# Performance work log

Hardware: AMD Instinct MI355X
Metric: run time of the kernel (lower is better)

The kernel has to match this reference:

```python
import jax, jax.numpy as jnp
import numpy as np

NUM_GROUPS = 16
MINIS_PER_GROUP = 16
MINIS_PER_TOK = 4
HIDDEN = 8192
N_TOKENS = 8192


def setup_inputs() -> dict:
    key = jax.random.key(0)
    k1, k2, k3 = jax.random.split(key, 3)
    hidden_states = jax.random.normal(k1, (N_TOKENS, HIDDEN), dtype=jnp.float32)
    # nn.Linear weight: [num_groups, hidden]
    group_gate_w = jax.random.normal(k2, (NUM_GROUPS, HIDDEN), dtype=jnp.float32) * 0.02
    # mini_gates parameter: [num_groups, hidden, minis_per_group]
    mini_gates = jax.random.normal(k3, (NUM_GROUPS, HIDDEN, MINIS_PER_GROUP), dtype=jnp.float32) * 0.02
    return {"hidden_states": hidden_states, "group_gate_w": group_gate_w, "mini_gates": mini_gates}


def reference(hidden_states, group_gate_w, mini_gates):
    # Tier 1: group gate
    group_logits = hidden_states @ group_gate_w.T                      # [N, G]
    group_probs = jax.nn.softmax(group_logits.astype(jnp.float32), axis=-1)
    top_group_probs = jnp.max(group_probs, axis=-1)                    # [N]
    top_group_indices = jnp.argmax(group_probs, axis=-1)               # [N]

    # Tier 2: per-token mini-gate. Instead of gathering a huge [N, H, E]
    # tensor (as the torch code does), compute logits for ALL groups
    # ([N, G, E] is tiny) and select the chosen group's row — same math.
    all_mini_logits = jnp.einsum('nh,ghe->nge', hidden_states, mini_gates)  # [N, G, E]
    mini_logits = jnp.take_along_axis(
        all_mini_logits, top_group_indices[:, None, None], axis=1
    )[:, 0, :]                                                         # [N, E]
    mini_probs = jax.nn.softmax(mini_logits.astype(jnp.float32), axis=-1)

    topk_mini_probs, topk_mini_indices = jax.lax.top_k(mini_probs, MINIS_PER_TOK)
    final_probs = top_group_probs[:, None] * topk_mini_probs
    final_probs = final_probs / jnp.sum(final_probs, axis=-1, keepdims=True)

    global_expert_indices = top_group_indices[:, None] * MINIS_PER_GROUP + topk_mini_indices

    group_aux_loss = jnp.sum(jnp.mean(group_probs, axis=0) ** 2)
    mini_aux_loss = jnp.sum(jnp.mean(mini_probs, axis=0) ** 2)
    total_aux_loss = group_aux_loss + mini_aux_loss

    return (final_probs.astype(hidden_states.dtype), global_expert_indices, total_aux_loss)
```

## Files before the change

kernel.cpp:

```cpp
#include <hip/hip_runtime.h>
#include <math.h>

#define N_TOK 8192
#define HID   8192
#define NG    16
#define NE    16
#define KC    256
#define NCHUNK (HID / KC)
#define TPB   16
#define TPW   2

#define OFF_CNT   0u
#define OFF_GSUM  64u
#define OFF_ESUM  128u
#define OFF_NTIL  192u
#define ZERO_BYTES 256u
#define OFF_BUCK  256u
#define OFF_SCHED (OFF_BUCK + NG*N_TOK*4)
#define OFF_MGT   (OFF_SCHED + 2048*4)

__device__ __forceinline__ void glds16(const float* gp, float* lp) {
    __builtin_amdgcn_global_load_lds(
        (const __attribute__((address_space(1))) void*)gp,
        (__attribute__((address_space(3))) void*)lp, 16, 0, 0);
}

#define RS_ROUND(o, half)                                                 \
  {                                                                       \
    const bool hi_ = (lane & (o)) != 0;                                   \
    _Pragma("unroll")                                                     \
    for (int i_ = 0; i_ < (half); ++i_) {                                 \
      float s_ = hi_ ? acc[i_] : acc[i_ + (half)];                        \
      float r_ = __shfl_xor(s_, (o));                                     \
      acc[i_] = (hi_ ? acc[i_ + (half)] : acc[i_]) + r_;                  \
    }                                                                     \
  }

__global__ __launch_bounds__(512, 4) void k_group(
    const float* __restrict__ hid, const float* __restrict__ gw,
    int* __restrict__ cnt, int* __restrict__ buckets, float* __restrict__ gsum)
{
    __shared__ float Wl[2][NG * KC];
    const int tid  = threadIdx.x;
    const int lane = tid & 63;
    const int wv   = tid >> 6;
    const int t0   = blockIdx.x * TPB + wv * TPW;
    const float* __restrict__ a0 = hid + (size_t)t0 * HID;

    #pragma unroll
    for (int j = 0; j < 2; ++j) {
        int g = wv * 2 + j;
        glds16(gw + (size_t)g * HID + 4 * lane, &Wl[0][g * KC]);
    }
    float4 areg[TPW];
    #pragma unroll
    for (int t = 0; t < TPW; ++t)
        areg[t] = *(const float4*)&a0[(size_t)t * HID + 4 * lane];

    float acc[32];
    #pragma unroll
    for (int i = 0; i < 32; ++i) acc[i] = 0.f;

    for (int c = 0; c < NCHUNK; ++c) {
        __syncthreads();
        float4 aC[TPW];
        #pragma unroll
        for (int t = 0; t < TPW; ++t) aC[t] = areg[t];
        if (c + 1 < NCHUNK) {
            const int kb = (c + 1) * KC;
            #pragma unroll
            for (int j = 0; j < 2; ++j) {
                int g = wv * 2 + j;
                glds16(gw + (size_t)g * HID + kb + 4 * lane, &Wl[(c + 1) & 1][g * KC]);
            }
            #pragma unroll
            for (int t = 0; t < TPW; ++t)
                areg[t] = *(const float4*)&a0[(size_t)t * HID + kb + 4 * lane];
        }
        const float* Wc = &Wl[c & 1][0];
        #pragma unroll
        for (int g = 0; g < NG; ++g) {
            float4 w = *(const float4*)&Wc[g * KC + 4 * lane];
            #pragma unroll
            for (int t = 0; t < TPW; ++t) {
                acc[t*16+g] = fmaf(aC[t].x, w.x, acc[t*16+g]);
                acc[t*16+g] = fmaf(aC[t].y, w.y, acc[t*16+g]);
                acc[t*16+g] = fmaf(aC[t].z, w.z, acc[t*16+g]);
                acc[t*16+g] = fmaf(aC[t].w, w.w, acc[t*16+g]);
            }
        }
    }

    #pragma unroll
    for (int i = 0; i < 32; ++i) acc[i] += __shfl_xor(acc[i], 32);
    RS_ROUND(16, 16) RS_ROUND(8, 8) RS_ROUND(4, 4) RS_ROUND(2, 2) RS_ROUND(1, 1)
    float v = acc[0];
    float mx = v;
    #pragma unroll
    for (int o = 8; o; o >>= 1) mx = fmaxf(mx, __shfl_xor(mx, o));
    float p = expf(v - mx);
    float s = p;
    #pragma unroll
    for (int o = 8; o; o >>= 1) s += __shfl_xor(s, o);
    p /= s;
    float x = p;
    x += __shfl_xor(x, 16);
    if (lane < 16) unsafeAtomicAdd(&gsum[lane], x);
    int gi = lane & 15; float bv = v;
    #pragma unroll
    for (int o = 8; o; o >>= 1) {
        float ov = __shfl_xor(bv, o);
        int   og = __shfl_xor(gi, o);
        if (ov > bv || (ov == bv && og < gi)) { bv = ov; gi = og; }
    }
    if (lane < 32 && (lane & 15) == 0) {
        int t = t0 + (lane >> 4);
        int pos = atomicAdd(&cnt[gi], 1);
        buckets[gi * N_TOK + pos] = t;
    }
}

__global__ __launch_bounds__(256) void k_tr(
    const float* __restrict__ mg, float* __restrict__ mgT)
{
    const int g  = blockIdx.x >> 7;
    const int kb = (blockIdx.x & 127) * 64;
    const int e  = threadIdx.x & 15;
    const int kq = threadIdx.x >> 4;
    const int k0 = kb + 4 * kq;
    const float* src = mg + (size_t)g * HID * NE;
    float4 v;
    v.x = src[(size_t)(k0 + 0) * NE + e];
    v.y = src[(size_t)(k0 + 1) * NE + e];
    v.z = src[(size_t)(k0 + 2) * NE + e];
    v.w = src[(size_t)(k0 + 3) * NE + e];
    *(float4*)&mgT[(size_t)(g * NE + e) * HID + k0] = v;
}

__global__ void k_sched(const int* __restrict__ cnt, int* __restrict__ sched,
                        int* __restrict__ ntile)
{
    __shared__ int pref[NG + 1];
    if (threadIdx.x == 0) {
        int s = 0;
        for (int g = 0; g < NG; ++g) { pref[g] = s; s += (cnt[g] + TPB - 1) / TPB; }
        pref[NG] = s; *ntile = s;
    }
    __syncthreads();
    int total = pref[NG];
    for (int i = threadIdx.x; i < total; i += blockDim.x) {
        int g = 0;
        while (g < NG - 1 && i >= pref[g + 1]) ++g;
        sched[i] = (g << 16) | (i - pref[g]);
    }
}

__global__ __launch_bounds__(512, 4) void k_mini(
    const float* __restrict__ hid, const float* __restrict__ mgT,
    const int* __restrict__ cnt, const int* __restrict__ buckets,
    const int* __restrict__ sched, const int* __restrict__ ntile,
    float* __restrict__ out, float* __restrict__ esum)
{
    if ((int)blockIdx.x >= *ntile) return;
    const int enc  = sched[blockIdx.x];
    const int g    = enc >> 16;
    const int tile = enc & 0xffff;
    const int n    = cnt[g] - tile * TPB;

    __shared__ float Wl[2][NE * KC];
    __shared__ int   rows[TPB];
    __shared__ float sm[256];
    const int tid  = threadIdx.x;
    const int lane = tid & 63;
    const int wv   = tid >> 6;
    const float* __restrict__ wg = mgT + (size_t)g * NE * HID;

    #pragma unroll
    for (int j = 0; j < 2; ++j) {
        int e = wv * 2 + j;
        glds16(wg + (size_t)e * HID + 4 * lane, &Wl[0][e * KC]);
    }
    if (tid < TPB)
        rows[tid] = buckets[g * N_TOK + tile * TPB + min(tid, n - 1)];
    __syncthreads();
    const float* at[TPW];
    #pragma unroll
    for (int t = 0; t < TPW; ++t) at[t] = hid + (size_t)rows[wv * TPW + t] * HID;

    float4 areg[TPW];
    #pragma unroll
    for (int t = 0; t < TPW; ++t)
        areg[t] = *(const float4*)&at[t][4 * lane];

    float acc[32];
    #pragma unroll
    for (int i = 0; i < 32; ++i) acc[i] = 0.f;

    for (int c = 0; c < NCHUNK; ++c) {
        __syncthreads();
        float4 aC[TPW];
        #pragma unroll
        for (int t = 0; t < TPW; ++t) aC[t] = areg[t];
        if (c + 1 < NCHUNK) {
            const int kb = (c + 1) * KC;
            #pragma unroll
            for (int j = 0; j < 2; ++j) {
                int e = wv * 2 + j;
                glds16(wg + (size_t)e * HID + kb + 4 * lane, &Wl[(c + 1) & 1][e * KC]);
            }
            #pragma unroll
            for (int t = 0; t < TPW; ++t)
                areg[t] = *(const float4*)&at[t][kb + 4 * lane];
        }
        const float* Wc = &Wl[c & 1][0];
        #pragma unroll
        for (int e = 0; e < NE; ++e) {
            float4 w = *(const float4*)&Wc[e * KC + 4 * lane];
            #pragma unroll
            for (int t = 0; t < TPW; ++t) {
                acc[t*16+e] = fmaf(aC[t].x, w.x, acc[t*16+e]);
                acc[t*16+e] = fmaf(aC[t].y, w.y, acc[t*16+e]);
                acc[t*16+e] = fmaf(aC[t].z, w.z, acc[t*16+e]);
                acc[t*16+e] = fmaf(aC[t].w, w.w, acc[t*16+e]);
            }
        }
    }

    #pragma unroll
    for (int i = 0; i < 32; ++i) acc[i] += __shfl_xor(acc[i], 32);
    RS_ROUND(16, 16) RS_ROUND(8, 8) RS_ROUND(4, 4) RS_ROUND(2, 2) RS_ROUND(1, 1)
    const int tl = wv * TPW + ((lane >> 4) & 1);
    float v = acc[0];
    float mx = v;
    #pragma unroll
    for (int o = 8; o; o >>= 1) mx = fmaxf(mx, __shfl_xor(mx, o));
    float p = expf(v - mx);
    float s = p;
    #pragma unroll
    for (int o = 8; o; o >>= 1) s += __shfl_xor(s, o);
    p /= s;
    float x = (tl < n) ? p : 0.f;
    x += __shfl_xor(x, 16);
    if (lane < 16) unsafeAtomicAdd(&esum[lane], x);

    if (lane < 32) sm[tl * 16 + (lane & 15)] = p;
    __syncthreads();
    if (tid < 256 && (tid & 15) == 0) {
        int tt = tid >> 4;
        if (tt < n) {
            float pe[NE];
            #pragma unroll
            for (int e = 0; e < NE; ++e) pe[e] = sm[tt * 16 + e];
            unsigned used = 0;
            float tv[4]; int ti[4];
            #pragma unroll
            for (int j = 0; j < 4; ++j) {
                float best = -1.f; int bi = 0;
                #pragma unroll
                for (int e = 0; e < NE; ++e)
                    if (!((used >> e) & 1u) && pe[e] > best) { best = pe[e]; bi = e; }
                used |= 1u << bi; tv[j] = best; ti[j] = bi;
            }
            float inv4 = 1.f / (tv[0] + tv[1] + tv[2] + tv[3]);
            int t = rows[tt];
            #pragma unroll
            for (int j = 0; j < 4; ++j) {
                out[t * 4 + j]             = tv[j] * inv4;
                out[N_TOK * 4 + t * 4 + j] = (float)(g * NE + ti[j]);
            }
        }
    }
}

__global__ void k_aux(const float* __restrict__ gsum, const float* __restrict__ esum,
                      float* __restrict__ out)
{
    if (threadIdx.x == 0) {
        float a = 0.f;
        for (int g = 0; g < NG; ++g) { float m = gsum[g] * (1.f / N_TOK); a += m * m; }
        for (int e = 0; e < NE; ++e) { float m = esum[e] * (1.f / N_TOK); a += m * m; }
        out[N_TOK * 8] = a;
    }
}

extern "C" void kernel_launch(void* const* d_in, const int* in_sizes, int n_in,
                              void* d_out, int out_size, void* d_ws, size_t ws_size,
                              hipStream_t stream) {
    const float* hid = (const float*)d_in[0];
    const float* gw  = (const float*)d_in[1];
    const float* mg  = (const float*)d_in[2];
    float* out = (float*)d_out;
    char*  ws  = (char*)d_ws;
    int*    cnt     = (int*)   (ws + OFF_CNT);
    float*  gsum    = (float*) (ws + OFF_GSUM);
    float*  esum    = (float*) (ws + OFF_ESUM);
    int*    ntile   = (int*)   (ws + OFF_NTIL);
    int*    buckets = (int*)   (ws + OFF_BUCK);
    int*    sched   = (int*)   (ws + OFF_SCHED);
    float*  mgT     = (float*) (ws + OFF_MGT);

    hipMemsetAsync(d_ws, 0, ZERO_BYTES, stream);

    k_tr<<<2048, 256, 0, stream>>>(mg, mgT);
    k_group<<<N_TOK / TPB, 512, 0, stream>>>(hid, gw, cnt, buckets, gsum);
    k_sched<<<1, 256, 0, stream>>>(cnt, sched, ntile);
    k_mini<<<N_TOK / TPB + NG, 512, 0, stream>>>(hid, mgT, cnt, buckets, sched, ntile, out, esum);
    k_aux<<<1, 64, 0, stream>>>(gsum, esum, out);
}
```

Baseline: 568.2 us.

## Read gate weights directly from global memory instead of LDS staging

```diff
diff --git a/kernel.cpp b/kernel.cpp
--- a/kernel.cpp
+++ b/kernel.cpp
@@ -18,12 +18,6 @@
 #define OFF_BUCK  256u
 #define OFF_SCHED (OFF_BUCK + NG*N_TOK*4)
 #define OFF_MGT   (OFF_SCHED + 2048*4)
-
-__device__ __forceinline__ void glds16(const float* gp, float* lp) {
-    __builtin_amdgcn_global_load_lds(
-        (const __attribute__((address_space(1))) void*)gp,
-        (__attribute__((address_space(3))) void*)lp, 16, 0, 0);
-}
 
 #define RS_ROUND(o, half)                                                 \
   {                                                                       \
@@ -40,47 +34,36 @@
     const float* __restrict__ hid, const float* __restrict__ gw,
     int* __restrict__ cnt, int* __restrict__ buckets, float* __restrict__ gsum)
 {
-    __shared__ float Wl[2][NG * KC];
     const int tid  = threadIdx.x;
     const int lane = tid & 63;
     const int wv   = tid >> 6;
     const int t0   = blockIdx.x * TPB + wv * TPW;
-    const float* __restrict__ a0 = hid + (size_t)t0 * HID;
-
-    #pragma unroll
-    for (int j = 0; j < 2; ++j) {
-        int g = wv * 2 + j;
-        glds16(gw + (size_t)g * HID + 4 * lane, &Wl[0][g * KC]);
-    }
+    const float* __restrict__ a0 = hid + (size_t)t0 * HID + 4 * lane;
+    const float* __restrict__ w0 = gw + 4 * lane;
+
     float4 areg[TPW];
     #pragma unroll
     for (int t = 0; t < TPW; ++t)
-        areg[t] = *(const float4*)&a0[(size_t)t * HID + 4 * lane];
+        areg[t] = *(const float4*)&a0[(size_t)t * HID];
 
     float acc[32];
     #pragma unroll
     for (int i = 0; i < 32; ++i) acc[i] = 0.f;
 
+    #pragma unroll 1
     for (int c = 0; c < NCHUNK; ++c) {
-        __syncthreads();
+        const int kb = c * KC;
         float4 aC[TPW];
         #pragma unroll
         for (int t = 0; t < TPW; ++t) aC[t] = areg[t];
         if (c + 1 < NCHUNK) {
-            const int kb = (c + 1) * KC;
-            #pragma unroll
-            for (int j = 0; j < 2; ++j) {
-                int g = wv * 2 + j;
-                glds16(gw + (size_t)g * HID + kb + 4 * lane, &Wl[(c + 1) & 1][g * KC]);
-            }
             #pragma unroll
             for (int t = 0; t < TPW; ++t)
-                areg[t] = *(const float4*)&a0[(size_t)t * HID + kb + 4 * lane];
-        }
-        const float* Wc = &Wl[c & 1][0];
+                areg[t] = *(const float4*)&a0[(size_t)t * HID + kb + KC];
+        }
         #pragma unroll
         for (int g = 0; g < NG; ++g) {
-            float4 w = *(const float4*)&Wc[g * KC + 4 * lane];
+            float4 w = *(const float4*)&w0[(size_t)g * HID + kb];
             #pragma unroll
             for (int t = 0; t < TPW; ++t) {
                 acc[t*16+g] = fmaf(aC[t].x, w.x, acc[t*16+g]);
@@ -89,6 +72,7 @@
                 acc[t*16+g] = fmaf(aC[t].w, w.w, acc[t*16+g]);
             }
         }
+        __builtin_amdgcn_s_barrier();
     }
 
     #pragma unroll
@@ -167,55 +151,44 @@
     const int tile = enc & 0xffff;
     const int n    = cnt[g] - tile * TPB;
 
-    __shared__ float Wl[2][NE * KC];
     __shared__ int   rows[TPB];
     __shared__ float sm[256];
     const int tid  = threadIdx.x;
     const int lane = tid & 63;
     const int wv   = tid >> 6;
-    const float* __restrict__ wg = mgT + (size_t)g * NE * HID;
-
-    #pragma unroll
-    for (int j = 0; j < 2; ++j) {
-        int e = wv * 2 + j;
-        glds16(wg + (size_t)e * HID + 4 * lane, &Wl[0][e * KC]);
-    }
+    const float* __restrict__ w0 = mgT + (size_t)g * NE * HID + 4 * lane;
+
     if (tid < TPB)
         rows[tid] = buckets[g * N_TOK + tile * TPB + min(tid, n - 1)];
     __syncthreads();
     const float* at[TPW];
     #pragma unroll
-    for (int t = 0; t < TPW; ++t) at[t] = hid + (size_t)rows[wv * TPW + t] * HID;
+    for (int t = 0; t < TPW; ++t)
+        at[t] = hid + (size_t)rows[wv * TPW + t] * HID + 4 * lane;
 
     float4 areg[TPW];
     #pragma unroll
     for (int t = 0; t < TPW; ++t)
-        areg[t] = *(const float4*)&at[t][4 * lane];
+        areg[t] = *(const float4*)&at[t][0];
 
     float acc[32];
     #pragma unroll
     for (int i = 0; i < 32; ++i) acc[i] = 0.f;
 
+    #pragma unroll 1
     for (int c = 0; c < NCHUNK; ++c) {
-        __syncthreads();
+        const int kb = c * KC;
         float4 aC[TPW];
         #pragma unroll
         for (int t = 0; t < TPW; ++t) aC[t] = areg[t];
         if (c + 1 < NCHUNK) {
-            const int kb = (c + 1) * KC;
-            #pragma unroll
-            for (int j = 0; j < 2; ++j) {
-                int e = wv * 2 + j;
-                glds16(wg + (size_t)e * HID + kb + 4 * lane, &Wl[(c + 1) & 1][e * KC]);
-            }
             #pragma unroll
             for (int t = 0; t < TPW; ++t)
-                areg[t] = *(const float4*)&at[t][kb + 4 * lane];
-        }
-        const float* Wc = &Wl[c & 1][0];
+                areg[t] = *(const float4*)&at[t][kb + KC];
+        }
         #pragma unroll
         for (int e = 0; e < NE; ++e) {
-            float4 w = *(const float4*)&Wc[e * KC + 4 * lane];
+            float4 w = *(const float4*)&w0[(size_t)e * HID + kb];
             #pragma unroll
             for (int t = 0; t < TPW; ++t) {
                 acc[t*16+e] = fmaf(aC[t].x, w.x, acc[t*16+e]);
@@ -224,6 +197,7 @@
                 acc[t*16+e] = fmaf(aC[t].w, w.w, acc[t*16+e]);
             }
         }
+        __builtin_amdgcn_s_barrier();
     }
 
     #pragma unroll
```

Result: slower. 589.1 us (+3.7%).
